# Kernel optimization log

Measured on AMD Instinct MI355X. Metric: run time of the kernel, lower is better.

Reference implementation:

```python
import jax, jax.numpy as jnp
import numpy as np

C = 1.0           # Poincare ball curvature magnitude (k = -1/c with c=1)
MIN_NORM = 1e-15
PROJ_EPS = 4e-3   # geoopt float32 boundary eps


def _artanh(x):
    return jnp.arctanh(jnp.clip(x, -1.0 + 1e-7, 1.0 - 1e-7))


def _norm(x):
    return jnp.maximum(jnp.linalg.norm(x, axis=-1, keepdims=True), MIN_NORM)


def mobius_matvec(W, x, c=C):
    # geoopt pmath.mobius_matvec with k=-c
    sc = jnp.sqrt(c)
    x_norm = _norm(x)
    Mx = x @ W.T
    Mx_norm = _norm(Mx)
    return jnp.tanh(Mx_norm / x_norm * _artanh(sc * x_norm)) * Mx / (Mx_norm * sc)


def mobius_add(x, y, c=C):
    x2 = jnp.sum(x * x, axis=-1, keepdims=True)
    y2 = jnp.sum(y * y, axis=-1, keepdims=True)
    xy = jnp.sum(x * y, axis=-1, keepdims=True)
    num = (1.0 + 2.0 * c * xy + c * y2) * x + (1.0 - c * x2) * y
    den = 1.0 + 2.0 * c * xy + c * c * x2 * y2
    return num / jnp.maximum(den, MIN_NORM)


def project(x, c=C):
    norm = _norm(x)
    maxnorm = (1.0 - PROJ_EPS) / jnp.sqrt(c)
    return jnp.where(norm > maxnorm, x / norm * maxnorm, x)


def expmap0(u, c=C):
    sc = jnp.sqrt(c)
    un = _norm(u)
    return jnp.tanh(sc * un) * u / (sc * un)


def mobius_linear(x, W, b, c=C):
    # hyperbolic_input=True, hyperbolic_bias=True, nonlin=None
    out = mobius_matvec(W, x, c)
    out = mobius_add(out, b, c)
    return project(out, c)


def setup_inputs() -> dict:
    key = jax.random.key(0)
    ks = jax.random.split(key, 7)
    N, D = 2048, 1024        # batch*tlen, input_size
    V = 32000                # output_size (vocab)
    SLEN, B, CV = 512, 32, 500
    hidden = jax.random.normal(ks[0], (N, D), jnp.float32) * 0.1
    hidden = project(hidden)
    attn = jax.random.uniform(ks[1], (N, SLEN), jnp.float32)
    src_map = jax.random.uniform(ks[2], (SLEN, B, CV), jnp.float32)
    W = jax.random.normal(ks[3], (V, D), jnp.float32) * 0.01
    b = expmap0(jax.random.normal(ks[4], (V,), jnp.float32) / 4.0)
    Wc = jax.random.normal(ks[5], (1, D), jnp.float32) * 0.01
    bc = expmap0(jax.random.normal(ks[6], (1,), jnp.float32) / 4.0)
    return {"hidden": hidden, "attn": attn, "src_map": src_map,
            "W": W, "b": b, "Wc": Wc, "bc": bc, "pad_idx": 1}


def reference(hidden, attn, src_map, W, b, Wc, bc, pad_idx):
    slen, batch, cvocab = src_map.shape
    logits = mobius_linear(hidden, W, b)                  # (N, V)
    logits = logits.at[:, pad_idx].set(-jnp.inf)
    prob = jax.nn.softmax(logits, axis=1)
    p_copy = jax.nn.sigmoid(mobius_linear(hidden, Wc, bc))  # (N, 1)
    out_prob = prob * (1.0 - p_copy)
    mul_attn = attn * p_copy                              # (N, slen)
    a = mul_attn.reshape(-1, batch, slen)                 # (tlen, batch, slen)
    copy_prob = jnp.einsum('tbs,sbc->tbc', a, src_map).reshape(-1, cvocab)
    return jnp.concatenate([out_prob, copy_prob], axis=1)
```

## Files before the change

kernel.cpp:

```cpp
#include <hip/hip_runtime.h>
#include <stdint.h>

#define N_ROWS   2048
#define D_IN     1024
#define V_OUT    32000
#define SLEN_C   512
#define BATCH_C  32
#define CVOC     500
#define OUT_COLS 32500

#define MIN_NORM_F 1e-15f
#define PROJ_EPS_F 4e-3f

typedef __bf16 bf16x8_t __attribute__((ext_vector_type(8)));
typedef float  f32x4_t  __attribute__((ext_vector_type(4)));

__device__ __forceinline__ unsigned short f2bf(float f) {
    uint32_t b = __float_as_uint(f);
    b += 0x7FFFu + ((b >> 16) & 1u);
    return (unsigned short)(b >> 16);
}
__device__ __forceinline__ float bf2f(unsigned short u) {
    return __uint_as_float(((uint32_t)u) << 16);
}
__device__ __forceinline__ float wave_sum(float v) {
#pragma unroll
    for (int off = 32; off > 0; off >>= 1) v += __shfl_down(v, off, 64);
    return v;
}

__device__ __forceinline__ void load_lds16(const void* g, void* l) {
    __builtin_amdgcn_global_load_lds(
        (const __attribute__((address_space(1))) void*)g,
        (__attribute__((address_space(3))) void*)l, 16, 0, 0);
}

__global__ __launch_bounds__(256)
void cast_f32_to_bf16(const float* __restrict__ src, unsigned short* __restrict__ dst, int n4) {
    int i = blockIdx.x * blockDim.x + threadIdx.x;
    int stride = gridDim.x * blockDim.x;
    for (; i < n4; i += stride) {
        float4 v = ((const float4*)src)[i];
        ushort4 o;
        o.x = f2bf(v.x); o.y = f2bf(v.y); o.z = f2bf(v.z); o.w = f2bf(v.w);
        ((ushort4*)dst)[i] = o;
    }
}

__global__ __launch_bounds__(1024)
void reduce_bsq(const float* __restrict__ bvec, float* __restrict__ out) {
    __shared__ float red[16];
    int tid = threadIdx.x;
    float s = 0.f;
    for (int i = tid; i < V_OUT; i += 1024) { float v = bvec[i]; s = fmaf(v, v, s); }
    s = wave_sum(s);
    int w = tid >> 6, l = tid & 63;
    if (l == 0) red[w] = s;
    __syncthreads();
    if (tid == 0) {
        float t = 0.f;
        for (int k = 0; k < 16; ++k) t += red[k];
        *out = t;
    }
}

__global__ __launch_bounds__(256)
void row_stats(const float* __restrict__ hidden, const float* __restrict__ Wc,
               const float* __restrict__ bc_in, float* __restrict__ g_arr,
               float* __restrict__ pc_arr) {
    __shared__ float red[8];
    const int n = blockIdx.x;
    const int tid = threadIdx.x;
    float4 hv = *(const float4*)(hidden + (size_t)n * D_IN + tid * 4);
    float4 wv = *(const float4*)(Wc + tid * 4);
    float s = hv.x * hv.x + hv.y * hv.y + hv.z * hv.z + hv.w * hv.w;
    float d = hv.x * wv.x + hv.y * wv.y + hv.z * wv.z + hv.w * wv.w;
    s = wave_sum(s); d = wave_sum(d);
    const int w = tid >> 6, l = tid & 63;
    if (l == 0) { red[w] = s; red[4 + w] = d; }
    __syncthreads();
    if (tid == 0) {
        float S  = red[0] + red[1] + red[2] + red[3];
        float Dc = red[4] + red[5] + red[6] + red[7];
        float xn = fmaxf(sqrtf(S), MIN_NORM_F);
        float xc = fminf(xn, 1.f - 1e-7f);
        float at = 0.5f * logf((1.f + xc) / (1.f - xc));
        float g = at / xn;
        float mxn = fmaxf(fabsf(Dc), MIN_NORM_F);
        float res = tanhf(mxn * g) * (Dc / mxn);
        float bcv = bc_in[0];
        float x2 = res * res, y2 = bcv * bcv, xyv = res * bcv;
        float num = (1.f + 2.f * xyv + y2) * res + (1.f - x2) * bcv;
        float dn  = fmaxf(1.f + 2.f * xyv + x2 * y2, MIN_NORM_F);
        float o = num / dn;
        float an = fmaxf(fabsf(o), MIN_NORM_F);
        float mxp = 1.f - PROJ_EPS_F;
        if (an > mxp) o = o / an * mxp;
        pc_arr[n] = 1.f / (1.f + expf(-o));
        g_arr[n]  = g;
    }
}

__global__ __launch_bounds__(256)
void gemm_bt_bf16(const unsigned short* __restrict__ A,
                  const unsigned short* __restrict__ B,
                  float* __restrict__ Cout)
{
    __shared__ unsigned short Als[128 * 64];
    __shared__ unsigned short Bls[128 * 64];
    const int tid  = threadIdx.x;
    const int wave = tid >> 6;
    const int lane = tid & 63;
    const int bn0 = blockIdx.x * 128;
    const int am0 = blockIdx.y * 128;

    const int srow  = lane >> 3;
    const int skoff = (lane & 7) * 8;
    const int fr = lane & 15;
    const int fk = (lane >> 4) * 8;
    const int wm = (wave >> 1) * 64;
    const int wn = (wave & 1) * 64;

    f32x4_t acc[4][4] = {};

    for (int kt = 0; kt < D_IN; kt += 64) {
#pragma unroll
        for (int q = 0; q < 4; ++q) {
            const int r0 = wave * 8 + q * 32;
            load_lds16(A + (size_t)(am0 + r0 + srow) * D_IN + kt + skoff, &Als[r0 * 64]);
            load_lds16(B + (size_t)(bn0 + r0 + srow) * D_IN + kt + skoff, &Bls[r0 * 64]);
        }
        __syncthreads();
#pragma unroll
        for (int kk = 0; kk < 64; kk += 32) {
            bf16x8_t af[4], bfr[4];
#pragma unroll
            for (int i = 0; i < 4; ++i)
                af[i] = *(const bf16x8_t*)&Als[(wm + i * 16 + fr) * 64 + kk + fk];
#pragma unroll
            for (int j = 0; j < 4; ++j)
                bfr[j] = *(const bf16x8_t*)&Bls[(wn + j * 16 + fr) * 64 + kk + fk];
#pragma unroll
            for (int i = 0; i < 4; ++i)
#pragma unroll
                for (int j = 0; j < 4; ++j)
                    acc[i][j] = __builtin_amdgcn_mfma_f32_16x16x32_bf16(af[i], bfr[j], acc[i][j], 0, 0, 0);
        }
        __syncthreads();
    }

    const int cm = (lane >> 4) * 4;
    const int cn = lane & 15;
#pragma unroll
    for (int i = 0; i < 4; ++i) {
#pragma unroll
        for (int j = 0; j < 4; ++j) {
            const int mg = am0 + wm + i * 16 + cm;
            const int ng = bn0 + wn + j * 16 + cn;
            float* cp = Cout + (size_t)mg * OUT_COLS + ng;
#pragma unroll
            for (int r = 0; r < 4; ++r) cp[(size_t)r * OUT_COLS] = acc[i][j][r];
        }
    }
}

__global__ __launch_bounds__(1024)
void softmax_epi(float* __restrict__ Cout, const float* __restrict__ bvec,
                 const float* __restrict__ g_arr, const float* __restrict__ pc_arr,
                 const float* __restrict__ sb_ptr, const int* __restrict__ pad_ptr) {
    __shared__ unsigned short mxls[V_OUT];
    __shared__ float red[32];
    __shared__ float bcast[4];
    const int n = blockIdx.x;
    const int tid = threadIdx.x;
    float* row = Cout + (size_t)n * OUT_COLS;
    const int pad = *pad_ptr;

    float s1 = 0.f, s2 = 0.f;
    for (int i = tid * 4; i < V_OUT; i += 4096) {
        float4 m  = *(const float4*)(row + i);
        float4 bv = *(const float4*)(bvec + i);
        s1 += m.x * m.x + m.y * m.y + m.z * m.z + m.w * m.w;
        s2 += m.x * bv.x + m.y * bv.y + m.z * bv.z + m.w * bv.w;
        ushort4 pk;
        pk.x = f2bf(m.x); pk.y = f2bf(m.y); pk.z = f2bf(m.z); pk.w = f2bf(m.w);
        *(ushort4*)&mxls[i] = pk;
    }
    s1 = wave_sum(s1); s2 = wave_sum(s2);
    const int w = tid >> 6, l = tid & 63;
    if (l == 0) { red[w] = s1; red[16 + w] = s2; }
    __syncthreads();
    if (tid == 0) {
        float a = 0.f, c2 = 0.f;
        for (int k = 0; k < 16; ++k) { a += red[k]; c2 += red[16 + k]; }
        bcast[0] = a; bcast[1] = c2;
    }
    __syncthreads();
    const float S1 = bcast[0], S2 = bcast[1];
    const float Sb = *sb_ptr;
    const float g  = g_arr[n];
    const float r   = fmaxf(sqrtf(S1), MIN_NORM_F);
    const float t   = tanhf(r * g);
    const float smv = t / r;
    const float x2 = smv * smv * S1;
    const float xy = smv * S2;
    const float y2 = Sb;
    const float den = fmaxf(1.f + 2.f * xy + x2 * y2, MIN_NORM_F);
    float P = (1.f + 2.f * xy + y2) * smv / den;
    float Q = (1.f - x2) / den;
    const float nrm = fmaxf(sqrtf(P * P * S1 + 2.f * P * Q * S2 + Q * Q * Sb), MIN_NORM_F);
    const float mxp = 1.f - PROJ_EPS_F;
    if (nrm > mxp) { const float f = mxp / nrm; P *= f; Q *= f; }

    float z = 0.f;
    for (int i = tid * 4; i < V_OUT; i += 4096) {
        ushort4 mu = *(const ushort4*)&mxls[i];
        float4 bv  = *(const float4*)(bvec + i);
        float e0 = __expf(P * bf2f(mu.x) + Q * bv.x);
        float e1 = __expf(P * bf2f(mu.y) + Q * bv.y);
        float e2 = __expf(P * bf2f(mu.z) + Q * bv.z);
        float e3 = __expf(P * bf2f(mu.w) + Q * bv.w);
        if (i + 0 == pad) e0 = 0.f;
        if (i + 1 == pad) e1 = 0.f;
        if (i + 2 == pad) e2 = 0.f;
        if (i + 3 == pad) e3 = 0.f;
        z += (e0 + e1) + (e2 + e3);
    }
    z = wave_sum(z);
    if (l == 0) red[w] = z;
    __syncthreads();
    if (tid == 0) {
        float a = 0.f;
        for (int k = 0; k < 16; ++k) a += red[k];
        bcast[2] = a;
    }
    __syncthreads();
    const float scale = (1.f - pc_arr[n]) / bcast[2];
    for (int i = tid * 4; i < V_OUT; i += 4096) {
        ushort4 mu = *(const ushort4*)&mxls[i];
        float4 bv  = *(const float4*)(bvec + i);
        float4 o;
        o.x = (i + 0 == pad) ? 0.f : __expf(P * bf2f(mu.x) + Q * bv.x) * scale;
        o.y = (i + 1 == pad) ? 0.f : __expf(P * bf2f(mu.y) + Q * bv.y) * scale;
        o.z = (i + 2 == pad) ? 0.f : __expf(P * bf2f(mu.z) + Q * bv.z) * scale;
        o.w = (i + 3 == pad) ? 0.f : __expf(P * bf2f(mu.w) + Q * bv.w) * scale;
        *(float4*)(row + i) = o;
    }
}

__global__ __launch_bounds__(128)
void copy_einsum(const float* __restrict__ attn, const float* __restrict__ src_map,
                 const float* __restrict__ pc_arr, float* __restrict__ Cout) {
    __shared__ float atile[32][128];
    const int tid = threadIdx.x;
    const int cc = blockIdx.x;
    const int b  = blockIdx.y;
    const int t0 = blockIdx.z * 32;
    const int c = cc * 128 + tid;
    const bool cv = (c < CVOC);

    float acc[32];
#pragma unroll
    for (int t = 0; t < 32; ++t) acc[t] = 0.f;

    for (int s0 = 0; s0 < SLEN_C; s0 += 128) {
        __syncthreads();
        for (int idx = tid; idx < 32 * 128; idx += 128) {
            const int t = idx >> 7, s = idx & 127;
            atile[t][s] = attn[(size_t)((t0 + t) * BATCH_C + b) * SLEN_C + s0 + s];
        }
        __syncthreads();
        for (int j = 0; j < 128; j += 4) {
            float sv0 = 0.f, sv1 = 0.f, sv2 = 0.f, sv3 = 0.f;
            if (cv) {
                const float* sp = src_map + (size_t)(s0 + j) * (BATCH_C * CVOC) + b * CVOC + c;
                sv0 = sp[0];
                sv1 = sp[BATCH_C * CVOC];
                sv2 = sp[2 * BATCH_C * CVOC];
                sv3 = sp[3 * BATCH_C * CVOC];
            }
#pragma unroll
            for (int t = 0; t < 32; ++t) {
                const float4 av = *(const float4*)&atile[t][j];
                acc[t] = fmaf(av.x, sv0, acc[t]);
                acc[t] = fmaf(av.y, sv1, acc[t]);
                acc[t] = fmaf(av.z, sv2, acc[t]);
                acc[t] = fmaf(av.w, sv3, acc[t]);
            }
        }
    }
    if (cv) {
#pragma unroll
        for (int t = 0; t < 32; ++t) {
            const int n = (t0 + t) * BATCH_C + b;
            Cout[(size_t)n * OUT_COLS + V_OUT + c] = acc[t] * pc_arr[n];
        }
    }
}

extern "C" void kernel_launch(void* const* d_in, const int* in_sizes, int n_in,
                              void* d_out, int out_size, void* d_ws, size_t ws_size,
                              hipStream_t stream) {
    const float* hidden  = (const float*)d_in[0];
    const float* attn    = (const float*)d_in[1];
    const float* src_map = (const float*)d_in[2];
    const float* W       = (const float*)d_in[3];
    const float* bvec    = (const float*)d_in[4];
    const float* Wc      = (const float*)d_in[5];
    const float* bc      = (const float*)d_in[6];
    const int*   padp    = (const int*)d_in[7];
    float* out = (float*)d_out;

    const int wb_elems = V_OUT * D_IN;
    const int hb_elems = N_ROWS * D_IN;
    unsigned short* Wb = (unsigned short*)d_ws;
    unsigned short* Hb = Wb + wb_elems;
    float* g_arr  = (float*)(Hb + hb_elems);
    float* pc_arr = g_arr + N_ROWS;
    float* sb     = pc_arr + N_ROWS;

    cast_f32_to_bf16<<<4000, 256, 0, stream>>>(W, Wb, wb_elems / 4);
    cast_f32_to_bf16<<<512, 256, 0, stream>>>(hidden, Hb, hb_elems / 4);
    reduce_bsq<<<1, 1024, 0, stream>>>(bvec, sb);
    row_stats<<<N_ROWS, 256, 0, stream>>>(hidden, Wc, bc, g_arr, pc_arr);

    dim3 ggrid(V_OUT / 128, N_ROWS / 128);
    gemm_bt_bf16<<<ggrid, 256, 0, stream>>>(Hb, Wb, out);

    softmax_epi<<<N_ROWS, 1024, 0, stream>>>(out, bvec, g_arr, pc_arr, sb, padp);

    dim3 egrid(4, BATCH_C, 2);
    copy_einsum<<<egrid, 128, 0, stream>>>(attn, src_map, pc_arr, out);
}
```

Baseline: 865.9 us.

## Store GEMM output as bf16, cache exp values in LDS, swizzle GEMM block order

The GEMM now writes bf16 results into the first half of each fp32 output row instead of full fp32, halving its store traffic. The softmax epilogue reads those bf16 values, computes the bias norm itself instead of calling a separate reduction kernel, and caches the exponentials as bf16 in LDS so the final pass only scales and writes. The GEMM grid is flattened and remapped into column strips so blocks that share W tiles run close together, for better L2 reuse. Risks: extra bf16 rounding on the exponentials, and reading and writing the same row in place relies on each row being fully loaded into LDS before any output is written.

```diff
diff --git a/kernel.cpp b/kernel.cpp
--- a/kernel.cpp
+++ b/kernel.cpp
@@ -14,6 +14,7 @@
 
 typedef __bf16 bf16x8_t __attribute__((ext_vector_type(8)));
 typedef float  f32x4_t  __attribute__((ext_vector_type(4)));
+typedef unsigned short ushort8_t __attribute__((ext_vector_type(8)));
 
 __device__ __forceinline__ unsigned short f2bf(float f) {
     uint32_t b = __float_as_uint(f);
@@ -44,23 +45,6 @@
         ushort4 o;
         o.x = f2bf(v.x); o.y = f2bf(v.y); o.z = f2bf(v.z); o.w = f2bf(v.w);
         ((ushort4*)dst)[i] = o;
-    }
-}
-
-__global__ __launch_bounds__(1024)
-void reduce_bsq(const float* __restrict__ bvec, float* __restrict__ out) {
-    __shared__ float red[16];
-    int tid = threadIdx.x;
-    float s = 0.f;
-    for (int i = tid; i < V_OUT; i += 1024) { float v = bvec[i]; s = fmaf(v, v, s); }
-    s = wave_sum(s);
-    int w = tid >> 6, l = tid & 63;
-    if (l == 0) red[w] = s;
-    __syncthreads();
-    if (tid == 0) {
-        float t = 0.f;
-        for (int k = 0; k < 16; ++k) t += red[k];
-        *out = t;
     }
 }
 
@@ -104,15 +88,18 @@
 __global__ __launch_bounds__(256)
 void gemm_bt_bf16(const unsigned short* __restrict__ A,
                   const unsigned short* __restrict__ B,
-                  float* __restrict__ Cout)
+                  unsigned short* __restrict__ Cb)
 {
     __shared__ unsigned short Als[128 * 64];
     __shared__ unsigned short Bls[128 * 64];
     const int tid  = threadIdx.x;
     const int wave = tid >> 6;
     const int lane = tid & 63;
-    const int bn0 = blockIdx.x * 128;
-    const int am0 = blockIdx.y * 128;
+    const int f   = blockIdx.x;
+    const int st  = f / 400;
+    const int loc = f - st * 400;
+    const int am0 = (loc & 15) * 128;
+    const int bn0 = (st * 25 + (loc >> 4)) * 128;
 
     const int srow  = lane >> 3;
     const int skoff = (lane & 7) * 8;
@@ -157,9 +144,10 @@
         for (int j = 0; j < 4; ++j) {
             const int mg = am0 + wm + i * 16 + cm;
             const int ng = bn0 + wn + j * 16 + cn;
-            float* cp = Cout + (size_t)mg * OUT_COLS + ng;
-#pragma unroll
-            for (int r = 0; r < 4; ++r) cp[(size_t)r * OUT_COLS] = acc[i][j][r];
+            unsigned short* cp = Cb + (size_t)mg * (OUT_COLS * 2) + ng;
+#pragma unroll
+            for (int r = 0; r < 4; ++r)
+                cp[(size_t)r * (OUT_COLS * 2)] = f2bf(acc[i][j][r]);
         }
     }
 }
@@ -167,64 +155,79 @@
 __global__ __launch_bounds__(1024)
 void softmax_epi(float* __restrict__ Cout, const float* __restrict__ bvec,
                  const float* __restrict__ g_arr, const float* __restrict__ pc_arr,
-                 const float* __restrict__ sb_ptr, const int* __restrict__ pad_ptr) {
+                 const int* __restrict__ pad_ptr) {
     __shared__ unsigned short mxls[V_OUT];
-    __shared__ float red[32];
+    __shared__ float red[48];
     __shared__ float bcast[4];
     const int n = blockIdx.x;
     const int tid = threadIdx.x;
     float* row = Cout + (size_t)n * OUT_COLS;
+    const unsigned short* rowb = (const unsigned short*)row;
     const int pad = *pad_ptr;
 
-    float s1 = 0.f, s2 = 0.f;
-    for (int i = tid * 4; i < V_OUT; i += 4096) {
-        float4 m  = *(const float4*)(row + i);
-        float4 bv = *(const float4*)(bvec + i);
-        s1 += m.x * m.x + m.y * m.y + m.z * m.z + m.w * m.w;
-        s2 += m.x * bv.x + m.y * bv.y + m.z * bv.z + m.w * bv.w;
-        ushort4 pk;
-        pk.x = f2bf(m.x); pk.y = f2bf(m.y); pk.z = f2bf(m.z); pk.w = f2bf(m.w);
-        *(ushort4*)&mxls[i] = pk;
-    }
-    s1 = wave_sum(s1); s2 = wave_sum(s2);
+    float s1 = 0.f, s2 = 0.f, s3 = 0.f;
+    for (int i = tid * 8; i < V_OUT; i += 8192) {
+        ushort8_t mu = *(const ushort8_t*)(rowb + i);
+        float4 b0 = *(const float4*)(bvec + i);
+        float4 b1 = *(const float4*)(bvec + i + 4);
+        float m0 = bf2f(mu[0]), m1 = bf2f(mu[1]), m2 = bf2f(mu[2]), m3 = bf2f(mu[3]);
+        float m4 = bf2f(mu[4]), m5 = bf2f(mu[5]), m6 = bf2f(mu[6]), m7 = bf2f(mu[7]);
+        s1 += (m0*m0 + m1*m1 + m2*m2 + m3*m3) + (m4*m4 + m5*m5 + m6*m6 + m7*m7);
+        s2 += (m0*b0.x + m1*b0.y + m2*b0.z + m3*b0.w) + (m4*b1.x + m5*b1.y + m6*b1.z + m7*b1.w);
+        s3 += (b0.x*b0.x + b0.y*b0.y + b0.z*b0.z + b0.w*b0.w)
+            + (b1.x*b1.x + b1.y*b1.y + b1.z*b1.z + b1.w*b1.w);
+        *(ushort8_t*)&mxls[i] = mu;
+    }
+    s1 = wave_sum(s1); s2 = wave_sum(s2); s3 = wave_sum(s3);
     const int w = tid >> 6, l = tid & 63;
-    if (l == 0) { red[w] = s1; red[16 + w] = s2; }
+    if (l == 0) { red[w] = s1; red[16 + w] = s2; red[32 + w] = s3; }
     __syncthreads();
     if (tid == 0) {
-        float a = 0.f, c2 = 0.f;
-        for (int k = 0; k < 16; ++k) { a += red[k]; c2 += red[16 + k]; }
-        bcast[0] = a; bcast[1] = c2;
-    }
-    __syncthreads();
-    const float S1 = bcast[0], S2 = bcast[1];
-    const float Sb = *sb_ptr;
-    const float g  = g_arr[n];
-    const float r   = fmaxf(sqrtf(S1), MIN_NORM_F);
-    const float t   = tanhf(r * g);
-    const float smv = t / r;
-    const float x2 = smv * smv * S1;
-    const float xy = smv * S2;
-    const float y2 = Sb;
-    const float den = fmaxf(1.f + 2.f * xy + x2 * y2, MIN_NORM_F);
-    float P = (1.f + 2.f * xy + y2) * smv / den;
-    float Q = (1.f - x2) / den;
-    const float nrm = fmaxf(sqrtf(P * P * S1 + 2.f * P * Q * S2 + Q * Q * Sb), MIN_NORM_F);
-    const float mxp = 1.f - PROJ_EPS_F;
-    if (nrm > mxp) { const float f = mxp / nrm; P *= f; Q *= f; }
+        float S1 = 0.f, S2 = 0.f, Sb = 0.f;
+        for (int k = 0; k < 16; ++k) { S1 += red[k]; S2 += red[16 + k]; Sb += red[32 + k]; }
+        const float g  = g_arr[n];
+        const float r   = fmaxf(sqrtf(S1), MIN_NORM_F);
+        const float t   = tanhf(r * g);
+        const float smv = t / r;
+        const float x2 = smv * smv * S1;
+        const float xy = smv * S2;
+        const float den = fmaxf(1.f + 2.f * xy + x2 * Sb, MIN_NORM_F);
+        float P = (1.f + 2.f * xy + Sb) * smv / den;
+        float Q = (1.f - x2) / den;
+        const float nrm = fmaxf(sqrtf(P * P * S1 + 2.f * P * Q * S2 + Q * Q * Sb), MIN_NORM_F);
+        const float mxp = 1.f - PROJ_EPS_F;
+        if (nrm > mxp) { const float fsc = mxp / nrm; P *= fsc; Q *= fsc; }
+        bcast[0] = P; bcast[1] = Q;
+    }
+    __syncthreads();
+    const float P = bcast[0], Q = bcast[1];
 
     float z = 0.f;
-    for (int i = tid * 4; i < V_OUT; i += 4096) {
-        ushort4 mu = *(const ushort4*)&mxls[i];
-        float4 bv  = *(const float4*)(bvec + i);
-        float e0 = __expf(P * bf2f(mu.x) + Q * bv.x);
-        float e1 = __expf(P * bf2f(mu.y) + Q * bv.y);
-        float e2 = __expf(P * bf2f(mu.z) + Q * bv.z);
-        float e3 = __expf(P * bf2f(mu.w) + Q * bv.w);
+    for (int i = tid * 8; i < V_OUT; i += 8192) {
+        ushort8_t mu = *(const ushort8_t*)&mxls[i];
+        float4 b0 = *(const float4*)(bvec + i);
+        float4 b1 = *(const float4*)(bvec + i + 4);
+        float e0 = __expf(fmaf(P, bf2f(mu[0]), Q * b0.x));
+        float e1 = __expf(fmaf(P, bf2f(mu[1]), Q * b0.y));
+        float e2 = __expf(fmaf(P, bf2f(mu[2]), Q * b0.z));
+        float e3 = __expf(fmaf(P, bf2f(mu[3]), Q * b0.w));
+        float e4 = __expf(fmaf(P, bf2f(mu[4]), Q * b1.x));
+        float e5 = __expf(fmaf(P, bf2f(mu[5]), Q * b1.y));
+        float e6 = __expf(fmaf(P, bf2f(mu[6]), Q * b1.z));
+        float e7 = __expf(fmaf(P, bf2f(mu[7]), Q * b1.w));
         if (i + 0 == pad) e0 = 0.f;
         if (i + 1 == pad) e1 = 0.f;
         if (i + 2 == pad) e2 = 0.f;
         if (i + 3 == pad) e3 = 0.f;
-        z += (e0 + e1) + (e2 + e3);
+        if (i + 4 == pad) e4 = 0.f;
+        if (i + 5 == pad) e5 = 0.f;
+        if (i + 6 == pad) e6 = 0.f;
+        if (i + 7 == pad) e7 = 0.f;
+        z += ((e0 + e1) + (e2 + e3)) + ((e4 + e5) + (e6 + e7));
+        ushort8_t eu;
+        eu[0] = f2bf(e0); eu[1] = f2bf(e1); eu[2] = f2bf(e2); eu[3] = f2bf(e3);
+        eu[4] = f2bf(e4); eu[5] = f2bf(e5); eu[6] = f2bf(e6); eu[7] = f2bf(e7);
+        *(ushort8_t*)&mxls[i] = eu;
     }
     z = wave_sum(z);
     if (l == 0) red[w] = z;
@@ -236,15 +239,16 @@
     }
     __syncthreads();
     const float scale = (1.f - pc_arr[n]) / bcast[2];
-    for (int i = tid * 4; i < V_OUT; i += 4096) {
-        ushort4 mu = *(const ushort4*)&mxls[i];
-        float4 bv  = *(const float4*)(bvec + i);
-        float4 o;
-        o.x = (i + 0 == pad) ? 0.f : __expf(P * bf2f(mu.x) + Q * bv.x) * scale;
-        o.y = (i + 1 == pad) ? 0.f : __expf(P * bf2f(mu.y) + Q * bv.y) * scale;
-        o.z = (i + 2 == pad) ? 0.f : __expf(P * bf2f(mu.z) + Q * bv.z) * scale;
-        o.w = (i + 3 == pad) ? 0.f : __expf(P * bf2f(mu.w) + Q * bv.w) * scale;
-        *(float4*)(row + i) = o;
+
+    for (int i = tid * 8; i < V_OUT; i += 8192) {
+        ushort8_t eu = *(const ushort8_t*)&mxls[i];
+        float4 o0, o1;
+        o0.x = bf2f(eu[0]) * scale; o0.y = bf2f(eu[1]) * scale;
+        o0.z = bf2f(eu[2]) * scale; o0.w = bf2f(eu[3]) * scale;
+        o1.x = bf2f(eu[4]) * scale; o1.y = bf2f(eu[5]) * scale;
+        o1.z = bf2f(eu[6]) * scale; o1.w = bf2f(eu[7]) * scale;
+        *(float4*)(row + i) = o0;
+        *(float4*)(row + i + 4) = o1;
     }
 }
 
@@ -317,17 +321,14 @@
     unsigned short* Hb = Wb + wb_elems;
     float* g_arr  = (float*)(Hb + hb_elems);
     float* pc_arr = g_arr + N_ROWS;
-    float* sb     = pc_arr + N_ROWS;
 
     cast_f32_to_bf16<<<4000, 256, 0, stream>>>(W, Wb, wb_elems / 4);
     cast_f32_to_bf16<<<512, 256, 0, stream>>>(hidden, Hb, hb_elems / 4);
-    reduce_bsq<<<1, 1024, 0, stream>>>(bvec, sb);
     row_stats<<<N_ROWS, 256, 0, stream>>>(hidden, Wc, bc, g_arr, pc_arr);
 
-    dim3 ggrid(V_OUT / 128, N_ROWS / 128);
-    gemm_bt_bf16<<<ggrid, 256, 0, stream>>>(Hb, Wb, out);
-
-    softmax_epi<<<N_ROWS, 1024, 0, stream>>>(out, bvec, g_arr, pc_arr, sb, padp);
+    gemm_bt_bf16<<<4000, 256, 0, stream>>>(Hb, Wb, (unsigned short*)out);
+
+    softmax_epi<<<N_ROWS, 1024, 0, stream>>>(out, bvec, g_arr, pc_arr, padp);
 
     dim3 egrid(4, BATCH_C, 2);
     copy_einsum<<<egrid, 128, 0, stream>>>(attn, src_map, pc_arr, out);
```

New measurement: 800.2 us. -7.6%, faster.
